# Performance work log

Hardware: AMD Instinct MI355X
Metric: run time of the kernel (lower is better)

The kernel has to match this reference:

```python
import jax, jax.numpy as jnp
import numpy as np

T, B, W, L = 64, 32, 1024, 4  # time, batch, hidden(=input) width, layers


def setup_inputs() -> dict:
    key = jax.random.key(0)
    ks = jax.random.split(key, 5)
    x = jax.random.normal(ks[0], (T, B, W), dtype=jnp.float32)
    resets = jax.random.randint(ks[1], (T, B), 0, 2).astype(bool)
    c0 = jnp.zeros((L, B, W), dtype=jnp.float32)
    h0 = jnp.zeros((L, B, W), dtype=jnp.float32)
    # Per-layer LSTM params (flax LSTMCell gate order: i, f, g, o concatenated).
    scale = 1.0 / np.sqrt(W)
    Wx = jax.random.normal(ks[2], (L, W, 4 * W), dtype=jnp.float32) * scale
    Wh = jax.random.normal(ks[3], (L, W, 4 * W), dtype=jnp.float32) * scale
    b = jnp.zeros((L, 4 * W), dtype=jnp.float32)
    return {"x": x, "resets": resets, "c0": c0, "h0": h0,
            "Wx": Wx, "Wh": Wh, "b": b}


def _lstm_scan(x, resets, c0, h0, Wx, Wh, b):
    num_layers = Wx.shape[0]

    def step(carry, xt):
        cs, hs = carry                      # each [L, B, W]
        ins, reset = xt                     # [B, W], [B]
        mask = reset[None, :, None]
        cs = jnp.where(mask, 0.0, cs)
        hs = jnp.where(mask, 0.0, hs)
        y = ins
        new_cs, new_hs = [], []
        for l in range(num_layers):
            gates = y @ Wx[l] + hs[l] @ Wh[l] + b[l]   # [B, 4W]
            i, f, g, o = jnp.split(gates, 4, axis=-1)
            c = jax.nn.sigmoid(f) * cs[l] + jax.nn.sigmoid(i) * jnp.tanh(g)
            h = jax.nn.sigmoid(o) * jnp.tanh(c)
            y = h
            new_cs.append(c)
            new_hs.append(h)
        return (jnp.stack(new_cs), jnp.stack(new_hs)), y

    (cs_f, hs_f), ys = jax.lax.scan(step, (c0, h0), (x, resets))
    return ys, cs_f, hs_f


def reference(x, resets, c0, h0, Wx, Wh, b):
    # ys: [T, B, W] stacked top-layer outputs; final carry also returned.
    return _lstm_scan(x, resets, c0, h0, Wx, Wh, b)
```

## Files before the change

### kernel.cpp

```cpp
#include <hip/hip_runtime.h>
#include <stdint.h>


typedef unsigned short u16;
typedef unsigned int u32;
typedef __attribute__((ext_vector_type(8))) short short8;
typedef __attribute__((ext_vector_type(4))) float f32x4;
typedef __attribute__((ext_vector_type(4))) unsigned int u32x4;

#define NT 64
#define NB 32
#define NW 1024
#define NLAY 4
#define G4 4096
#define POISON 0xAAAAAAAAu

#define HIST_OFF 0
#define RMASK_OFF 17104896
#define MODE_OFF 17113088

__device__ __forceinline__ float bf2f(u16 u) {
  union { u32 i; float f; } v; v.i = ((u32)u) << 16; return v.f;
}
__device__ __forceinline__ u16 f2bf(float f) {
  union { float f; u32 i; } v; v.f = f;
  u32 b = v.i;
  return (u16)((b + 0x7FFFu + ((b >> 16) & 1u)) >> 16);
}
__device__ __forceinline__ float sigmoidf_(float x) { return 1.f / (1.f + __expf(-x)); }
__device__ __forceinline__ float tanhfast(float x) {
  float cx = fminf(fmaxf(x, -15.f), 15.f);
  float e = __expf(2.f * cx);
  return (e - 1.f) / (e + 1.f);
}
union CastU { u32x4 u; short8 s; };
__device__ __forceinline__ short8 as_s8(u32x4 v) { CastU c; c.u = v; return c.s; }
__device__ __forceinline__ u32x4 as_u4(short8 v) { CastU c; c.s = v; return c.u; }

__device__ __forceinline__ void poll_half(const u16* rowA, const u16* rowB, u32x4 r[16]) {
  for (;;) {
#pragma unroll
    for (int q = 0; q < 8; ++q) {
      asm volatile("global_load_dwordx4 %0, %1, off sc0 sc1" : "=v"(r[q]) : "v"(rowA + q * 32));
      asm volatile("global_load_dwordx4 %0, %1, off sc0 sc1" : "=v"(r[8 + q]) : "v"(rowB + q * 32));
    }
    asm volatile("s_waitcnt vmcnt(0)"
                 : "+v"(r[0]), "+v"(r[1]), "+v"(r[2]), "+v"(r[3]), "+v"(r[4]), "+v"(r[5]),
                   "+v"(r[6]), "+v"(r[7]), "+v"(r[8]), "+v"(r[9]), "+v"(r[10]), "+v"(r[11]),
                   "+v"(r[12]), "+v"(r[13]), "+v"(r[14]), "+v"(r[15])
                 :
                 : "memory");
    bool ok = true;
    const u16* probe = rowA;
    bool have = false;
#pragma unroll
    for (int c = 0; c < 16; ++c) {
      bool f = (r[c].x != POISON) && (r[c].y != POISON) && (r[c].z != POISON) && (r[c].w != POISON);
      if (!f && !have) { probe = (c < 8) ? (rowA + c * 32) : (rowB + (c - 8) * 32); have = true; }
      ok &= f;
    }
    if (ok) return;
    for (;;) {
      __builtin_amdgcn_s_sleep(4);
      u32x4 v;
      asm volatile("global_load_dwordx4 %0, %1, off sc0 sc1" : "=v"(v) : "v"(probe));
      asm volatile("s_waitcnt vmcnt(0)" : "+v"(v) : : "memory");
      if ((v.x != POISON) && (v.y != POISON) && (v.z != POISON) && (v.w != POISON)) break;
    }
  }
}

__global__ void lstm_setup(const void* __restrict__ x, const void* __restrict__ resets,
                           int* __restrict__ modes, int* __restrict__ rmask) {
  __shared__ int votes_bf16, bad_int, bad_float;
  __shared__ int sm_rmode;
  int tid = threadIdx.x;
  if (tid == 0) { votes_bf16 = 0; bad_int = 0; bad_float = 0; }
  __syncthreads();
  {
    u32 w = ((const u32*)x)[tid];
    int e = (int)((w >> 7) & 0xFFu);
    if (e >= 100 && e <= 140) atomicAdd(&votes_bf16, 1);
  }
  if (tid < 128) {
    u32 r = ((const u32*)resets)[tid];
    if (r > 1u) atomicAdd(&bad_int, 1);
    if (r != 0u && r != 0x3F800000u) atomicAdd(&bad_float, 1);
  }
  __syncthreads();
  if (tid == 0) {
    int mbf = (votes_bf16 >= 192) ? 1 : 0;
    int rmode;
    if (bad_int == 0) rmode = 1;
    else if (bad_float == 0) rmode = 2;
    else rmode = 0;
    modes[0] = mbf;
    modes[1] = rmode;
    sm_rmode = rmode;
  }
  __syncthreads();
  int rmode = sm_rmode;
#pragma unroll
  for (int k = 0; k < 8; ++k) {
    int idx = tid * 8 + k;
    int val;
    if (rmode == 1) val = (((const int*)resets)[idx] != 0);
    else if (rmode == 2) val = (((const u32*)resets)[idx] != 0u);
    else val = (((const unsigned char*)resets)[idx] != 0);
    rmask[idx] = val;
  }
}

__global__ void lstm_poison(u32* __restrict__ hist32) {
  int g = (blockIdx.x * 256 + threadIdx.x) * 4;
  int l = g >> 20;
  int r = g & 1048575;
  u32x4 v = {POISON, POISON, POISON, POISON};
  *(u32x4*)(hist32 + ((size_t)l * 65 + 1) * 16384 + r) = v;
}

template <bool BF16>
__global__ void lstm_prep(const void* __restrict__ h0, const int* __restrict__ modes,
                          u16* __restrict__ hist) {
  if ((modes[0] != 0) != BF16) return;
  int idx = blockIdx.x * 256 + threadIdx.x;
  int l = idx >> 15;
  int rem = idx & 32767;
  float hv;
  if (BF16) hv = bf2f(((const u16*)h0)[idx]);
  else      hv = ((const float*)h0)[idx];
  hist[(size_t)l * (65 * NB * NW) + rem] = f2bf(hv);
}

template <bool BF16>
__global__ __launch_bounds__(256, 1) void lstm_main(
    const void* __restrict__ xv, const void* __restrict__ Wxv,
    const void* __restrict__ Whv, const void* __restrict__ biasv,
    const void* __restrict__ c0v,
    void* __restrict__ outv, const int* __restrict__ modes,
    const int* __restrict__ rmask, u16* __restrict__ hist) {
  if ((modes[0] != 0) != BF16) return;

  const int l = blockIdx.x >> 6;
  const int s = blockIdx.x & 63;
  const int hb = s * 16;
  const int tid = threadIdx.x;
  const int wave = tid >> 6;
  const int lane = tid & 63;
  const bool xpart = (wave < 2);
  const int krel = (wave & 1) * 512;
  const int lrow = lane & 15;
  const int lk8 = (lane >> 4) * 8;

  const int eb = tid >> 3;
  const int n0 = (tid & 7) * 2;
  const int emt = eb >> 4, er = eb & 15;

  __shared__ float red[4][2][4][16][17];

  short8 wfrag[4][16];
  {
    const size_t base = (size_t)l * NW * G4;
#pragma unroll
    for (int g = 0; g < 4; ++g) {
#pragma unroll
      for (int kt = 0; kt < 16; ++kt) {
        size_t off = base + (size_t)(krel + kt * 32 + lk8) * G4 + (size_t)(g * 1024 + hb + lrow);
        short8 v;
        if (BF16) {
          const u16* p = (xpart ? (const u16*)Wxv : (const u16*)Whv) + off;
#pragma unroll
          for (int j = 0; j < 8; ++j) v[j] = (short)p[(size_t)j * G4];
        } else {
          const float* p = (xpart ? (const float*)Wxv : (const float*)Whv) + off;
#pragma unroll
          for (int j = 0; j < 8; ++j) v[j] = (short)f2bf(p[(size_t)j * G4]);
        }
        wfrag[g][kt] = v;
      }
    }
  }

  float bias_r[4][2];
#pragma unroll
  for (int g = 0; g < 4; ++g)
#pragma unroll
    for (int j = 0; j < 2; ++j) {
      int bidx = l * G4 + g * 1024 + hb + n0 + j;
      bias_r[g][j] = BF16 ? bf2f(((const u16*)biasv)[bidx]) : ((const float*)biasv)[bidx];
    }

  float creg[2] = {0.f, 0.f};

#pragma unroll 1
  for (int t = 0; t < NT; ++t) {
    const u16* srcH = hist + ((size_t)l * 65 + t) * (NB * NW);
    const u16* srcY = hist + ((size_t)(l - 1) * 65 + (t + 1)) * (NB * NW);
    const u16* srcXb = (const u16*)xv + (size_t)t * NB * NW;
    const float* srcXf = (const float*)xv + (size_t)t * NB * NW;

    int rm0 = 0, rm1 = 0;
    if (!xpart) {
      rm0 = rmask[t * NB + lrow];
      rm1 = rmask[t * NB + 16 + lrow];
    }

    f32x4 acc[2][4];
    f32x4 zf = {0.f, 0.f, 0.f, 0.f};
#pragma unroll
    for (int mt = 0; mt < 2; ++mt)
#pragma unroll
      for (int g = 0; g < 4; ++g) acc[mt][g] = zf;

#pragma unroll
    for (int half = 0; half < 2; ++half) {
      u32x4 r[16];
      const int kbase = krel + half * 256 + lk8;
      if (xpart) {
        if (l > 0) {
          poll_half(srcY + (size_t)lrow * NW + kbase, srcY + (size_t)(lrow + 16) * NW + kbase, r);
        } else if (BF16) {
#pragma unroll
          for (int q = 0; q < 8; ++q) {
            r[q] = *(const u32x4*)(srcXb + (size_t)lrow * NW + kbase + q * 32);
            r[8 + q] = *(const u32x4*)(srcXb + (size_t)(lrow + 16) * NW + kbase + q * 32);
          }
        } else {
#pragma unroll
          for (int q = 0; q < 8; ++q) {
            const f32x4* p0 = (const f32x4*)(srcXf + (size_t)lrow * NW + kbase + q * 32);
            const f32x4* p1 = (const f32x4*)(srcXf + (size_t)(lrow + 16) * NW + kbase + q * 32);
            f32x4 x0a = p0[0], x0b = p0[1], x1a = p1[0], x1b = p1[1];
            short8 a0, a1;
#pragma unroll
            for (int j = 0; j < 4; ++j) {
              a0[j] = (short)f2bf(x0a[j]);
              a0[j + 4] = (short)f2bf(x0b[j]);
              a1[j] = (short)f2bf(x1a[j]);
              a1[j + 4] = (short)f2bf(x1b[j]);
            }
            r[q] = as_u4(a0);
            r[8 + q] = as_u4(a1);
          }
        }
      } else {
        poll_half(srcH + (size_t)lrow * NW + kbase, srcH + (size_t)(lrow + 16) * NW + kbase, r);
        u32x4 z4 = {0u, 0u, 0u, 0u};
        if (rm0) {
#pragma unroll
          for (int q = 0; q < 8; ++q) r[q] = z4;
        }
        if (rm1) {
#pragma unroll
          for (int q = 0; q < 8; ++q) r[8 + q] = z4;
        }
      }
#pragma unroll
      for (int q = 0; q < 8; ++q) {
        const int kt = half * 8 + q;
#pragma unroll
        for (int g = 0; g < 4; ++g) {
          acc[0][g] = __builtin_amdgcn_mfma_f32_16x16x32_bf16(as_s8(r[q]), wfrag[g][kt], acc[0][g], 0, 0, 0);
          acc[1][g] = __builtin_amdgcn_mfma_f32_16x16x32_bf16(as_s8(r[8 + q]), wfrag[g][kt], acc[1][g], 0, 0, 0);
        }
      }
    }

#pragma unroll
    for (int mt = 0; mt < 2; ++mt)
#pragma unroll
      for (int g = 0; g < 4; ++g)
#pragma unroll
        for (int r2 = 0; r2 < 4; ++r2)
          red[wave][mt][g][(lane >> 4) * 4 + r2][lrow] = acc[mt][g][r2];
    __syncthreads();

    {
      int rm = rmask[t * NB + eb];
      float hn[2];
#pragma unroll
      for (int j = 0; j < 2; ++j) {
        int n = n0 + j;
        float gv[4];
#pragma unroll
        for (int g = 0; g < 4; ++g)
          gv[g] = red[0][emt][g][er][n] + red[1][emt][g][er][n] +
                  red[2][emt][g][er][n] + red[3][emt][g][er][n] + bias_r[g][j];
        float c_old = creg[j];
        if (t == 0) {
          int cidx = (l * NB + eb) * NW + hb + n;
          c_old = BF16 ? bf2f(((const u16*)c0v)[cidx]) : ((const float*)c0v)[cidx];
        }
        if (rm) c_old = 0.f;
        float ci = sigmoidf_(gv[0]);
        float cf = sigmoidf_(gv[1]);
        float cg = tanhfast(gv[2]);
        float co = sigmoidf_(gv[3]);
        float cn = cf * c_old + ci * cg;
        hn[j] = co * tanhfast(cn);
        creg[j] = cn;
      }
      u32 hp = (u32)f2bf(hn[0]) | ((u32)f2bf(hn[1]) << 16);
      size_t hoff = ((size_t)l * 65 + (t + 1)) * (NB * NW) + (size_t)eb * NW + hb + n0;
      __hip_atomic_store((u32*)(hist + hoff), hp, __ATOMIC_RELAXED, __HIP_MEMORY_SCOPE_AGENT);
      if (l == NLAY - 1) {
        size_t oy = ((size_t)t * NB + eb) * NW + hb + n0;
        if (BF16) ((u32*)outv)[oy >> 1] = hp;
        else { ((float*)outv)[oy] = hn[0]; ((float*)outv)[oy + 1] = hn[1]; }
      }
      if (t == NT - 1) {
        size_t oc = (size_t)NT * NB * NW + ((size_t)l * NB + eb) * NW + hb + n0;
        size_t oh = oc + (size_t)NLAY * NB * NW;
        if (BF16) {
          u32 cp = (u32)f2bf(creg[0]) | ((u32)f2bf(creg[1]) << 16);
          ((u32*)outv)[oc >> 1] = cp;
          ((u32*)outv)[oh >> 1] = hp;
        } else {
          ((float*)outv)[oc] = creg[0];
          ((float*)outv)[oc + 1] = creg[1];
          ((float*)outv)[oh] = hn[0];
          ((float*)outv)[oh + 1] = hn[1];
        }
      }
    }
    __syncthreads();
  }
}

extern "C" void kernel_launch(void* const* d_in, const int* in_sizes, int n_in,
                              void* d_out, int out_size, void* d_ws, size_t ws_size,
                              hipStream_t stream) {
  const void* x = d_in[0];
  const void* resets = d_in[1];
  const void* c0 = d_in[2];
  const void* h0 = d_in[3];
  const void* Wx = d_in[4];
  const void* Wh = d_in[5];
  const void* bias = d_in[6];

  char* ws = (char*)d_ws;
  u16* hist = (u16*)(ws + HIST_OFF);
  int* rmask = (int*)(ws + RMASK_OFF);
  int* modes = (int*)(ws + MODE_OFF);

  lstm_setup<<<1, 256, 0, stream>>>(x, resets, modes, rmask);
  lstm_poison<<<4096, 256, 0, stream>>>((u32*)hist);
  lstm_prep<true><<<512, 256, 0, stream>>>(h0, modes, hist);
  lstm_prep<false><<<512, 256, 0, stream>>>(h0, modes, hist);
  lstm_main<true><<<256, 256, 0, stream>>>(x, Wx, Wh, bias, c0, d_out, modes, rmask, hist);
  lstm_main<false><<<256, 256, 0, stream>>>(x, Wx, Wh, bias, c0, d_out, modes, rmask, hist);
}
```

Baseline: 1.035 ms.

## Replace poison-value data polling with per-block ready flags

Each block now publishes a per-timestep ready flag after its hidden-state stores have completed. Consumer waves spin on the 32 flags covering their K-slice before doing a single plain load of the history data, instead of repeatedly reloading the data and checking it for a poison sentinel. This removes the separate kernel that filled the history buffer with poison and cuts redundant wide reloads while spinning. The cost is an extra dependent round trip on the recurrent critical path: producers must store, wait, barrier and then set the flag, and consumers must see the flag before loading.

After: 1.096 ms. +5.8%, slower.

```diff
diff --git a/kernel.cpp b/kernel.cpp
--- a/kernel.cpp
+++ b/kernel.cpp
@@ -13,11 +13,12 @@
 #define NW 1024
 #define NLAY 4
 #define G4 4096
-#define POISON 0xAAAAAAAAu
 
 #define HIST_OFF 0
 #define RMASK_OFF 17104896
 #define MODE_OFF 17113088
+#define FLAG_OFF 17113344
+#define FLAG_PER_L 4160
 
 __device__ __forceinline__ float bf2f(u16 u) {
   union { u32 i; float f; } v; v.i = ((u32)u) << 16; return v.f;
@@ -37,41 +38,33 @@
 __device__ __forceinline__ short8 as_s8(u32x4 v) { CastU c; c.u = v; return c.s; }
 __device__ __forceinline__ u32x4 as_u4(short8 v) { CastU c; c.s = v; return c.u; }
 
-__device__ __forceinline__ void poll_half(const u16* rowA, const u16* rowB, u32x4 r[16]) {
+__device__ __forceinline__ void load_half(const u16* rowA, const u16* rowB, u32x4 r[16]) {
+#pragma unroll
+  for (int q = 0; q < 8; ++q) {
+    asm volatile("global_load_dwordx4 %0, %1, off sc0 sc1" : "=v"(r[q]) : "v"(rowA + q * 32));
+    asm volatile("global_load_dwordx4 %0, %1, off sc0 sc1" : "=v"(r[8 + q]) : "v"(rowB + q * 32));
+  }
+  asm volatile("s_waitcnt vmcnt(0)"
+               : "+v"(r[0]), "+v"(r[1]), "+v"(r[2]), "+v"(r[3]), "+v"(r[4]), "+v"(r[5]),
+                 "+v"(r[6]), "+v"(r[7]), "+v"(r[8]), "+v"(r[9]), "+v"(r[10]), "+v"(r[11]),
+                 "+v"(r[12]), "+v"(r[13]), "+v"(r[14]), "+v"(r[15])
+               :
+               : "memory");
+}
+
+__device__ __forceinline__ void poll_ready(const u32* fp) {
   for (;;) {
-#pragma unroll
-    for (int q = 0; q < 8; ++q) {
-      asm volatile("global_load_dwordx4 %0, %1, off sc0 sc1" : "=v"(r[q]) : "v"(rowA + q * 32));
-      asm volatile("global_load_dwordx4 %0, %1, off sc0 sc1" : "=v"(r[8 + q]) : "v"(rowB + q * 32));
-    }
-    asm volatile("s_waitcnt vmcnt(0)"
-                 : "+v"(r[0]), "+v"(r[1]), "+v"(r[2]), "+v"(r[3]), "+v"(r[4]), "+v"(r[5]),
-                   "+v"(r[6]), "+v"(r[7]), "+v"(r[8]), "+v"(r[9]), "+v"(r[10]), "+v"(r[11]),
-                   "+v"(r[12]), "+v"(r[13]), "+v"(r[14]), "+v"(r[15])
-                 :
-                 : "memory");
-    bool ok = true;
-    const u16* probe = rowA;
-    bool have = false;
-#pragma unroll
-    for (int c = 0; c < 16; ++c) {
-      bool f = (r[c].x != POISON) && (r[c].y != POISON) && (r[c].z != POISON) && (r[c].w != POISON);
-      if (!f && !have) { probe = (c < 8) ? (rowA + c * 32) : (rowB + (c - 8) * 32); have = true; }
-      ok &= f;
-    }
-    if (ok) return;
-    for (;;) {
-      __builtin_amdgcn_s_sleep(4);
-      u32x4 v;
-      asm volatile("global_load_dwordx4 %0, %1, off sc0 sc1" : "=v"(v) : "v"(probe));
-      asm volatile("s_waitcnt vmcnt(0)" : "+v"(v) : : "memory");
-      if ((v.x != POISON) && (v.y != POISON) && (v.z != POISON) && (v.w != POISON)) break;
-    }
+    u32 f;
+    asm volatile("global_load_dword %0, %1, off sc0 sc1" : "=v"(f) : "v"(fp));
+    asm volatile("s_waitcnt vmcnt(0)" : "+v"(f) : : "memory");
+    if (__all(f != 0)) return;
+    __builtin_amdgcn_s_sleep(1);
   }
 }
 
 __global__ void lstm_setup(const void* __restrict__ x, const void* __restrict__ resets,
-                           int* __restrict__ modes, int* __restrict__ rmask) {
+                           int* __restrict__ modes, int* __restrict__ rmask,
+                           u32* __restrict__ flags) {
   __shared__ int votes_bf16, bad_int, bad_float;
   __shared__ int sm_rmode;
   int tid = threadIdx.x;
@@ -109,14 +102,9 @@
     else val = (((const unsigned char*)resets)[idx] != 0);
     rmask[idx] = val;
   }
-}
-
-__global__ void lstm_poison(u32* __restrict__ hist32) {
-  int g = (blockIdx.x * 256 + threadIdx.x) * 4;
-  int l = g >> 20;
-  int r = g & 1048575;
-  u32x4 v = {POISON, POISON, POISON, POISON};
-  *(u32x4*)(hist32 + ((size_t)l * 65 + 1) * 16384 + r) = v;
+  for (int i = 0; i < 65; ++i) flags[tid * 65 + i] = 0;
+  __syncthreads();
+  flags[(tid >> 6) * FLAG_PER_L + (tid & 63)] = 1;
 }
 
 template <bool BF16>
@@ -138,7 +126,8 @@
     const void* __restrict__ Whv, const void* __restrict__ biasv,
     const void* __restrict__ c0v,
     void* __restrict__ outv, const int* __restrict__ modes,
-    const int* __restrict__ rmask, u16* __restrict__ hist) {
+    const int* __restrict__ rmask, u16* __restrict__ hist,
+    u32* __restrict__ flags) {
   if ((modes[0] != 0) != BF16) return;
 
   const int l = blockIdx.x >> 6;
@@ -158,6 +147,11 @@
 
   __shared__ float red[4][2][4][16][17];
 
+  const u32* fpoll = xpart ? (l > 0 ? flags + (size_t)(l - 1) * FLAG_PER_L : nullptr)
+                           : flags + (size_t)l * FLAG_PER_L;
+  const int fslice = (krel >> 4) + (lane & 31);
+  u32* fset = flags + (size_t)l * FLAG_PER_L + 64 + s;
+
   short8 wfrag[4][16];
   {
     const size_t base = (size_t)l * NW * G4;
@@ -205,6 +199,12 @@
       rm1 = rmask[t * NB + 16 + lrow];
     }
 
+    if (xpart) {
+      if (l > 0) poll_ready(fpoll + (size_t)(t + 1) * 64 + fslice);
+    } else {
+      poll_ready(fpoll + (size_t)t * 64 + fslice);
+    }
+
     f32x4 acc[2][4];
     f32x4 zf = {0.f, 0.f, 0.f, 0.f};
 #pragma unroll
@@ -218,7 +218,7 @@
       const int kbase = krel + half * 256 + lk8;
       if (xpart) {
         if (l > 0) {
-          poll_half(srcY + (size_t)lrow * NW + kbase, srcY + (size_t)(lrow + 16) * NW + kbase, r);
+          load_half(srcY + (size_t)lrow * NW + kbase, srcY + (size_t)(lrow + 16) * NW + kbase, r);
         } else if (BF16) {
 #pragma unroll
           for (int q = 0; q < 8; ++q) {
@@ -244,7 +244,7 @@
           }
         }
       } else {
-        poll_half(srcH + (size_t)lrow * NW + kbase, srcH + (size_t)(lrow + 16) * NW + kbase, r);
+        load_half(srcH + (size_t)lrow * NW + kbase, srcH + (size_t)(lrow + 16) * NW + kbase, r);
         u32x4 z4 = {0u, 0u, 0u, 0u};
         if (rm0) {
 #pragma unroll
@@ -275,6 +275,7 @@
           red[wave][mt][g][(lane >> 4) * 4 + r2][lrow] = acc[mt][g][r2];
     __syncthreads();
 
+    u32 hp;
     {
       int rm = rmask[t * NB + eb];
       float hn[2];
@@ -300,9 +301,10 @@
         hn[j] = co * tanhfast(cn);
         creg[j] = cn;
       }
-      u32 hp = (u32)f2bf(hn[0]) | ((u32)f2bf(hn[1]) << 16);
+      hp = (u32)f2bf(hn[0]) | ((u32)f2bf(hn[1]) << 16);
       size_t hoff = ((size_t)l * 65 + (t + 1)) * (NB * NW) + (size_t)eb * NW + hb + n0;
-      __hip_atomic_store((u32*)(hist + hoff), hp, __ATOMIC_RELAXED, __HIP_MEMORY_SCOPE_AGENT);
+      u32* hptr = (u32*)(hist + hoff);
+      asm volatile("global_store_dword %0, %1, off sc0 sc1" : : "v"(hptr), "v"(hp) : "memory");
       if (l == NLAY - 1) {
         size_t oy = ((size_t)t * NB + eb) * NW + hb + n0;
         if (BF16) ((u32*)outv)[oy >> 1] = hp;
@@ -323,7 +325,13 @@
         }
       }
     }
+
+    asm volatile("s_waitcnt vmcnt(0)" : : : "memory");
     __syncthreads();
+    if (tid == 0) {
+      asm volatile("global_store_dword %0, %1, off sc0 sc1" : : "v"(fset), "v"(1u) : "memory");
+    }
+    fset += 64;
   }
 }
 
@@ -342,11 +350,11 @@
   u16* hist = (u16*)(ws + HIST_OFF);
   int* rmask = (int*)(ws + RMASK_OFF);
   int* modes = (int*)(ws + MODE_OFF);
-
-  lstm_setup<<<1, 256, 0, stream>>>(x, resets, modes, rmask);
-  lstm_poison<<<4096, 256, 0, stream>>>((u32*)hist);
+  u32* flags = (u32*)(ws + FLAG_OFF);
+
+  lstm_setup<<<1, 256, 0, stream>>>(x, resets, modes, rmask, flags);
   lstm_prep<true><<<512, 256, 0, stream>>>(h0, modes, hist);
   lstm_prep<false><<<512, 256, 0, stream>>>(h0, modes, hist);
-  lstm_main<true><<<256, 256, 0, stream>>>(x, Wx, Wh, bias, c0, d_out, modes, rmask, hist);
-  lstm_main<false><<<256, 256, 0, stream>>>(x, Wx, Wh, bias, c0, d_out, modes, rmask, hist);
-}
+  lstm_main<true><<<256, 256, 0, stream>>>(x, Wx, Wh, bias, c0, d_out, modes, rmask, hist, flags);
+  lstm_main<false><<<256, 256, 0, stream>>>(x, Wx, Wh, bias, c0, d_out, modes, rmask, hist, flags);
+}
```

## Double-buffer reduction LDS and retry only stale chunks when polling

Applied to the files above, without the earlier changes.

The LDS reduction buffer is double-buffered by timestep parity, which lets the trailing __syncthreads at the end of each timestep be removed so waves can start polling the next step earlier. The polling routine now keeps a per-chunk stale bitmask and reloads only the chunks that are still stale, instead of reloading all chunks after a single-probe sleep loop. It sleeps only when every chunk is stale and uses wave-wide votes for loop exit. This shortens the latency on the recurrent critical path, at the cost of twice the LDS and reliance on the double buffer to avoid write-after-read races between steps.

After: 1.052 ms. Within noise of the previous version (+1.6%).

```diff
diff --git a/kernel.cpp b/kernel.cpp
--- a/kernel.cpp
+++ b/kernel.cpp
@@ -37,35 +37,42 @@
 __device__ __forceinline__ short8 as_s8(u32x4 v) { CastU c; c.u = v; return c.s; }
 __device__ __forceinline__ u32x4 as_u4(short8 v) { CastU c; c.s = v; return c.u; }
 
+__device__ __forceinline__ bool fresh4(u32x4 v) {
+  return (v.x != POISON) && (v.y != POISON) && (v.z != POISON) && (v.w != POISON);
+}
+
+#define WAITCNT_ALL(r)                                                                        \
+  asm volatile("s_waitcnt vmcnt(0)"                                                           \
+               : "+v"(r[0]), "+v"(r[1]), "+v"(r[2]), "+v"(r[3]), "+v"(r[4]), "+v"(r[5]),      \
+                 "+v"(r[6]), "+v"(r[7]), "+v"(r[8]), "+v"(r[9]), "+v"(r[10]), "+v"(r[11]),    \
+                 "+v"(r[12]), "+v"(r[13]), "+v"(r[14]), "+v"(r[15])                           \
+               :                                                                              \
+               : "memory")
+
 __device__ __forceinline__ void poll_half(const u16* rowA, const u16* rowB, u32x4 r[16]) {
-  for (;;) {
-#pragma unroll
-    for (int q = 0; q < 8; ++q) {
-      asm volatile("global_load_dwordx4 %0, %1, off sc0 sc1" : "=v"(r[q]) : "v"(rowA + q * 32));
-      asm volatile("global_load_dwordx4 %0, %1, off sc0 sc1" : "=v"(r[8 + q]) : "v"(rowB + q * 32));
-    }
-    asm volatile("s_waitcnt vmcnt(0)"
-                 : "+v"(r[0]), "+v"(r[1]), "+v"(r[2]), "+v"(r[3]), "+v"(r[4]), "+v"(r[5]),
-                   "+v"(r[6]), "+v"(r[7]), "+v"(r[8]), "+v"(r[9]), "+v"(r[10]), "+v"(r[11]),
-                   "+v"(r[12]), "+v"(r[13]), "+v"(r[14]), "+v"(r[15])
-                 :
-                 : "memory");
-    bool ok = true;
-    const u16* probe = rowA;
-    bool have = false;
+#pragma unroll
+  for (int q = 0; q < 8; ++q) {
+    asm volatile("global_load_dwordx4 %0, %1, off sc0 sc1" : "=v"(r[q]) : "v"(rowA + q * 32));
+    asm volatile("global_load_dwordx4 %0, %1, off sc0 sc1" : "=v"(r[8 + q]) : "v"(rowB + q * 32));
+  }
+  WAITCNT_ALL(r);
+  u32 stale = 0;
+#pragma unroll
+  for (int c = 0; c < 16; ++c)
+    if (!fresh4(r[c])) stale |= (1u << c);
+  while (__any(stale != 0)) {
+    if (__all(stale == 0xFFFFu)) __builtin_amdgcn_s_sleep(2);
 #pragma unroll
     for (int c = 0; c < 16; ++c) {
-      bool f = (r[c].x != POISON) && (r[c].y != POISON) && (r[c].z != POISON) && (r[c].w != POISON);
-      if (!f && !have) { probe = (c < 8) ? (rowA + c * 32) : (rowB + (c - 8) * 32); have = true; }
-      ok &= f;
-    }
-    if (ok) return;
-    for (;;) {
-      __builtin_amdgcn_s_sleep(4);
-      u32x4 v;
-      asm volatile("global_load_dwordx4 %0, %1, off sc0 sc1" : "=v"(v) : "v"(probe));
-      asm volatile("s_waitcnt vmcnt(0)" : "+v"(v) : : "memory");
-      if ((v.x != POISON) && (v.y != POISON) && (v.z != POISON) && (v.w != POISON)) break;
+      if (stale & (1u << c)) {
+        const u16* p = (c < 8) ? (rowA + c * 32) : (rowB + (c - 8) * 32);
+        asm volatile("global_load_dwordx4 %0, %1, off sc0 sc1" : "=v"(r[c]) : "v"(p));
+      }
+    }
+    WAITCNT_ALL(r);
+#pragma unroll
+    for (int c = 0; c < 16; ++c) {
+      if ((stale & (1u << c)) && fresh4(r[c])) stale &= ~(1u << c);
     }
   }
 }
@@ -156,7 +163,7 @@
   const int n0 = (tid & 7) * 2;
   const int emt = eb >> 4, er = eb & 15;
 
-  __shared__ float red[4][2][4][16][17];
+  __shared__ float red[2][4][2][4][16][17];
 
   short8 wfrag[4][16];
   {
@@ -194,6 +201,7 @@
 
 #pragma unroll 1
   for (int t = 0; t < NT; ++t) {
+    const int buf = t & 1;
     const u16* srcH = hist + ((size_t)l * 65 + t) * (NB * NW);
     const u16* srcY = hist + ((size_t)(l - 1) * 65 + (t + 1)) * (NB * NW);
     const u16* srcXb = (const u16*)xv + (size_t)t * NB * NW;
@@ -272,7 +280,7 @@
       for (int g = 0; g < 4; ++g)
 #pragma unroll
         for (int r2 = 0; r2 < 4; ++r2)
-          red[wave][mt][g][(lane >> 4) * 4 + r2][lrow] = acc[mt][g][r2];
+          red[buf][wave][mt][g][(lane >> 4) * 4 + r2][lrow] = acc[mt][g][r2];
     __syncthreads();
 
     {
@@ -284,8 +292,8 @@
         float gv[4];
 #pragma unroll
         for (int g = 0; g < 4; ++g)
-          gv[g] = red[0][emt][g][er][n] + red[1][emt][g][er][n] +
-                  red[2][emt][g][er][n] + red[3][emt][g][er][n] + bias_r[g][j];
+          gv[g] = red[buf][0][emt][g][er][n] + red[buf][1][emt][g][er][n] +
+                  red[buf][2][emt][g][er][n] + red[buf][3][emt][g][er][n] + bias_r[g][j];
         float c_old = creg[j];
         if (t == 0) {
           int cidx = (l * NB + eb) * NW + hb + n;
@@ -323,7 +331,6 @@
         }
       }
     }
-    __syncthreads();
   }
 }
 
```

## Decouple input-projection and recurrent waves with LDS flag pipeline

Applied to the files above, without the earlier changes.

Splits each block into two wave groups: the y/x-projection waves run ahead through timesteps independently, writing partial sums into double-buffered LDS slots and signalling via LDS counters. The h-recurrent waves compute the Wh product, wait for both partial sums, and do the elementwise cell update, replacing the per-step block-wide barriers. This lets the input-projection GEMM for step t+1 overlap the recurrent critical path. It adds spin-wait flag synchronization with memory-ordering risk and uses different poll sleep intervals for the two groups.

Result: slower. 1.086 ms (+4.9%).

```diff
diff --git a/kernel.cpp b/kernel.cpp
--- a/kernel.cpp
+++ b/kernel.cpp
@@ -37,6 +37,22 @@
 __device__ __forceinline__ short8 as_s8(u32x4 v) { CastU c; c.u = v; return c.s; }
 __device__ __forceinline__ u32x4 as_u4(short8 v) { CastU c; c.s = v; return c.u; }
 
+__device__ __forceinline__ bool fresh4(u32x4 v) {
+  return (v.x != POISON) && (v.y != POISON) && (v.z != POISON) && (v.w != POISON);
+}
+
+__device__ __forceinline__ void lds_bump(int* p) {
+  __threadfence_block();
+  if ((threadIdx.x & 63) == 0)
+    __hip_atomic_fetch_add(p, 1, __ATOMIC_RELAXED, __HIP_MEMORY_SCOPE_WORKGROUP);
+}
+__device__ __forceinline__ void lds_wait(int* p, int want) {
+  while (__hip_atomic_load(p, __ATOMIC_RELAXED, __HIP_MEMORY_SCOPE_WORKGROUP) < want)
+    __builtin_amdgcn_s_sleep(1);
+  __threadfence_block();
+}
+
+template <int SLP>
 __device__ __forceinline__ void poll_half(const u16* rowA, const u16* rowB, u32x4 r[16]) {
   for (;;) {
 #pragma unroll
@@ -61,7 +77,7 @@
     }
     if (ok) return;
     for (;;) {
-      __builtin_amdgcn_s_sleep(4);
+      __builtin_amdgcn_s_sleep(SLP);
       u32x4 v;
       asm volatile("global_load_dwordx4 %0, %1, off sc0 sc1" : "=v"(v) : "v"(probe));
       asm volatile("s_waitcnt vmcnt(0)" : "+v"(v) : : "memory");
@@ -147,16 +163,16 @@
   const int tid = threadIdx.x;
   const int wave = tid >> 6;
   const int lane = tid & 63;
-  const bool xpart = (wave < 2);
+  const bool ypart = (wave < 2);
   const int krel = (wave & 1) * 512;
   const int lrow = lane & 15;
   const int lk8 = (lane >> 4) * 8;
 
-  const int eb = tid >> 3;
-  const int n0 = (tid & 7) * 2;
-  const int emt = eb >> 4, er = eb & 15;
-
-  __shared__ float red[4][2][4][16][17];
+  __shared__ float yred[2][2][2][4][16][17];
+  __shared__ float hred[2][2][2][4][16][17];
+  __shared__ int yflag, hflag, edone;
+
+  if (tid == 0) { yflag = 0; hflag = 0; edone = 0; }
 
   short8 wfrag[4][16];
   {
@@ -168,11 +184,11 @@
         size_t off = base + (size_t)(krel + kt * 32 + lk8) * G4 + (size_t)(g * 1024 + hb + lrow);
         short8 v;
         if (BF16) {
-          const u16* p = (xpart ? (const u16*)Wxv : (const u16*)Whv) + off;
+          const u16* p = (ypart ? (const u16*)Wxv : (const u16*)Whv) + off;
 #pragma unroll
           for (int j = 0; j < 8; ++j) v[j] = (short)p[(size_t)j * G4];
         } else {
-          const float* p = (xpart ? (const float*)Wxv : (const float*)Whv) + off;
+          const float* p = (ypart ? (const float*)Wxv : (const float*)Whv) + off;
 #pragma unroll
           for (int j = 0; j < 8; ++j) v[j] = (short)f2bf(p[(size_t)j * G4]);
         }
@@ -180,45 +196,29 @@
       }
     }
   }
-
-  float bias_r[4][2];
-#pragma unroll
-  for (int g = 0; g < 4; ++g)
-#pragma unroll
-    for (int j = 0; j < 2; ++j) {
-      int bidx = l * G4 + g * 1024 + hb + n0 + j;
-      bias_r[g][j] = BF16 ? bf2f(((const u16*)biasv)[bidx]) : ((const float*)biasv)[bidx];
-    }
-
-  float creg[2] = {0.f, 0.f};
-
+  __syncthreads();
+
+  if (ypart) {
 #pragma unroll 1
-  for (int t = 0; t < NT; ++t) {
-    const u16* srcH = hist + ((size_t)l * 65 + t) * (NB * NW);
-    const u16* srcY = hist + ((size_t)(l - 1) * 65 + (t + 1)) * (NB * NW);
-    const u16* srcXb = (const u16*)xv + (size_t)t * NB * NW;
-    const float* srcXf = (const float*)xv + (size_t)t * NB * NW;
-
-    int rm0 = 0, rm1 = 0;
-    if (!xpart) {
-      rm0 = rmask[t * NB + lrow];
-      rm1 = rmask[t * NB + 16 + lrow];
-    }
-
-    f32x4 acc[2][4];
-    f32x4 zf = {0.f, 0.f, 0.f, 0.f};
-#pragma unroll
-    for (int mt = 0; mt < 2; ++mt)
-#pragma unroll
-      for (int g = 0; g < 4; ++g) acc[mt][g] = zf;
-
-#pragma unroll
-    for (int half = 0; half < 2; ++half) {
-      u32x4 r[16];
-      const int kbase = krel + half * 256 + lk8;
-      if (xpart) {
+    for (int t = 0; t < NT; ++t) {
+      const int slot = t & 1;
+      const u16* srcY = hist + ((size_t)(l - 1) * 65 + (t + 1)) * (NB * NW);
+      const u16* srcXb = (const u16*)xv + (size_t)t * NB * NW;
+      const float* srcXf = (const float*)xv + (size_t)t * NB * NW;
+
+      f32x4 acc[2][4];
+      f32x4 zf = {0.f, 0.f, 0.f, 0.f};
+#pragma unroll
+      for (int mt = 0; mt < 2; ++mt)
+#pragma unroll
+        for (int g = 0; g < 4; ++g) acc[mt][g] = zf;
+
+#pragma unroll
+      for (int half = 0; half < 2; ++half) {
+        u32x4 r[16];
+        const int kbase = krel + half * 256 + lk8;
         if (l > 0) {
-          poll_half(srcY + (size_t)lrow * NW + kbase, srcY + (size_t)(lrow + 16) * NW + kbase, r);
+          poll_half<16>(srcY + (size_t)lrow * NW + kbase, srcY + (size_t)(lrow + 16) * NW + kbase, r);
         } else if (BF16) {
 #pragma unroll
           for (int q = 0; q < 8; ++q) {
@@ -243,8 +243,64 @@
             r[8 + q] = as_u4(a1);
           }
         }
-      } else {
-        poll_half(srcH + (size_t)lrow * NW + kbase, srcH + (size_t)(lrow + 16) * NW + kbase, r);
+#pragma unroll
+        for (int q = 0; q < 8; ++q) {
+          const int kt = half * 8 + q;
+#pragma unroll
+          for (int g = 0; g < 4; ++g) {
+            acc[0][g] = __builtin_amdgcn_mfma_f32_16x16x32_bf16(as_s8(r[q]), wfrag[g][kt], acc[0][g], 0, 0, 0);
+            acc[1][g] = __builtin_amdgcn_mfma_f32_16x16x32_bf16(as_s8(r[8 + q]), wfrag[g][kt], acc[1][g], 0, 0, 0);
+          }
+        }
+      }
+
+      if (t >= 2) lds_wait(&edone, 2 * (t - 1));
+#pragma unroll
+      for (int mt = 0; mt < 2; ++mt)
+#pragma unroll
+        for (int g = 0; g < 4; ++g)
+#pragma unroll
+          for (int e = 0; e < 4; ++e)
+            yred[slot][wave][mt][g][(lane >> 4) * 4 + e][lrow] = acc[mt][g][e];
+      lds_bump(&yflag);
+    }
+  } else {
+    const int hw = wave - 2;
+    const int tid2 = tid - 128;
+    const int eb = tid2 >> 2;
+    const int eu = (tid2 & 3) * 4;
+    const int emt = eb >> 4, er = eb & 15;
+
+    float bias_r[4][4];
+#pragma unroll
+    for (int g = 0; g < 4; ++g)
+#pragma unroll
+      for (int j = 0; j < 4; ++j) {
+        int bidx = l * G4 + g * 1024 + hb + eu + j;
+        bias_r[g][j] = BF16 ? bf2f(((const u16*)biasv)[bidx]) : ((const float*)biasv)[bidx];
+      }
+
+    float creg[4] = {0.f, 0.f, 0.f, 0.f};
+
+#pragma unroll 1
+    for (int t = 0; t < NT; ++t) {
+      const int slot = t & 1;
+      const u16* srcH = hist + ((size_t)l * 65 + t) * (NB * NW);
+      int rm0 = rmask[t * NB + lrow];
+      int rm1 = rmask[t * NB + 16 + lrow];
+
+      f32x4 acc[2][4];
+      f32x4 zf = {0.f, 0.f, 0.f, 0.f};
+#pragma unroll
+      for (int mt = 0; mt < 2; ++mt)
+#pragma unroll
+        for (int g = 0; g < 4; ++g) acc[mt][g] = zf;
+
+#pragma unroll
+      for (int half = 0; half < 2; ++half) {
+        u32x4 r[16];
+        const int kbase = krel + half * 256 + lk8;
+        poll_half<4>(srcH + (size_t)lrow * NW + kbase, srcH + (size_t)(lrow + 16) * NW + kbase, r);
         u32x4 z4 = {0u, 0u, 0u, 0u};
         if (rm0) {
 #pragma unroll
@@ -254,76 +310,90 @@
 #pragma unroll
           for (int q = 0; q < 8; ++q) r[8 + q] = z4;
         }
+#pragma unroll
+        for (int q = 0; q < 8; ++q) {
+          const int kt = half * 8 + q;
+#pragma unroll
+          for (int g = 0; g < 4; ++g) {
+            acc[0][g] = __builtin_amdgcn_mfma_f32_16x16x32_bf16(as_s8(r[q]), wfrag[g][kt], acc[0][g], 0, 0, 0);
+            acc[1][g] = __builtin_amdgcn_mfma_f32_16x16x32_bf16(as_s8(r[8 + q]), wfrag[g][kt], acc[1][g], 0, 0, 0);
+          }
+        }
       }
-#pragma unroll
-      for (int q = 0; q < 8; ++q) {
-        const int kt = half * 8 + q;
-#pragma unroll
-        for (int g = 0; g < 4; ++g) {
-          acc[0][g] = __builtin_amdgcn_mfma_f32_16x16x32_bf16(as_s8(r[q]), wfrag[g][kt], acc[0][g], 0, 0, 0);
-          acc[1][g] = __builtin_amdgcn_mfma_f32_16x16x32_bf16(as_s8(r[8 + q]), wfrag[g][kt], acc[1][g], 0, 0, 0);
+
+      if (t >= 2) lds_wait(&edone, 2 * (t - 1));
+#pragma unroll
+      for (int mt = 0; mt < 2; ++mt)
+#pragma unroll
+        for (int g = 0; g < 4; ++g)
+#pragma unroll
+          for (int e = 0; e < 4; ++e)
+            hred[slot][hw][mt][g][(lane >> 4) * 4 + e][lrow] = acc[mt][g][e];
+      lds_bump(&hflag);
+
+      lds_wait(&hflag, 2 * (t + 1));
+      lds_wait(&yflag, 2 * (t + 1));
+
+      {
+        int rm = rmask[t * NB + eb];
+        float hn[4];
+#pragma unroll
+        for (int j = 0; j < 4; ++j) {
+          int n = eu + j;
+          float gv[4];
+#pragma unroll
+          for (int g = 0; g < 4; ++g)
+            gv[g] = yred[slot][0][emt][g][er][n] + yred[slot][1][emt][g][er][n] +
+                    hred[slot][0][emt][g][er][n] + hred[slot][1][emt][g][er][n] + bias_r[g][j];
+          float c_old = creg[j];
+          if (t == 0) {
+            int cidx = (l * NB + eb) * NW + hb + n;
+            c_old = BF16 ? bf2f(((const u16*)c0v)[cidx]) : ((const float*)c0v)[cidx];
+          }
+          if (rm) c_old = 0.f;
+          float ci = sigmoidf_(gv[0]);
+          float cf = sigmoidf_(gv[1]);
+          float cg = tanhfast(gv[2]);
+          float co = sigmoidf_(gv[3]);
+          float cn = cf * c_old + ci * cg;
+          hn[j] = co * tanhfast(cn);
+          creg[j] = cn;
+        }
+        u32 hp0 = (u32)f2bf(hn[0]) | ((u32)f2bf(hn[1]) << 16);
+        u32 hp1 = (u32)f2bf(hn[2]) | ((u32)f2bf(hn[3]) << 16);
+        size_t hoff = ((size_t)l * 65 + (t + 1)) * (NB * NW) + (size_t)eb * NW + hb + eu;
+        u32* hptr = (u32*)(hist + hoff);
+        __hip_atomic_store(hptr, hp0, __ATOMIC_RELAXED, __HIP_MEMORY_SCOPE_AGENT);
+        __hip_atomic_store(hptr + 1, hp1, __ATOMIC_RELAXED, __HIP_MEMORY_SCOPE_AGENT);
+        if (l == NLAY - 1) {
+          size_t oy = ((size_t)t * NB + eb) * NW + hb + eu;
+          if (BF16) {
+            ((u32*)outv)[oy >> 1] = hp0;
+            ((u32*)outv)[(oy >> 1) + 1] = hp1;
+          } else {
+            float* op = (float*)outv + oy;
+            op[0] = hn[0]; op[1] = hn[1]; op[2] = hn[2]; op[3] = hn[3];
+          }
+        }
+        if (t == NT - 1) {
+          size_t oc = (size_t)NT * NB * NW + ((size_t)l * NB + eb) * NW + hb + eu;
+          size_t oh = oc + (size_t)NLAY * NB * NW;
+          if (BF16) {
+            u32 cp0 = (u32)f2bf(creg[0]) | ((u32)f2bf(creg[1]) << 16);
+            u32 cp1 = (u32)f2bf(creg[2]) | ((u32)f2bf(creg[3]) << 16);
+            ((u32*)outv)[oc >> 1] = cp0;
+            ((u32*)outv)[(oc >> 1) + 1] = cp1;
+            ((u32*)outv)[oh >> 1] = hp0;
+            ((u32*)outv)[(oh >> 1) + 1] = hp1;
+          } else {
+            float* ov = (float*)outv;
+            ov[oc + 0] = creg[0]; ov[oc + 1] = creg[1]; ov[oc + 2] = creg[2]; ov[oc + 3] = creg[3];
+            ov[oh + 0] = hn[0]; ov[oh + 1] = hn[1]; ov[oh + 2] = hn[2]; ov[oh + 3] = hn[3];
+          }
         }
       }
-    }
-
-#pragma unroll
-    for (int mt = 0; mt < 2; ++mt)
-#pragma unroll
-      for (int g = 0; g < 4; ++g)
-#pragma unroll
-        for (int r2 = 0; r2 < 4; ++r2)
-          red[wave][mt][g][(lane >> 4) * 4 + r2][lrow] = acc[mt][g][r2];
-    __syncthreads();
-
-    {
-      int rm = rmask[t * NB + eb];
-      float hn[2];
-#pragma unroll
-      for (int j = 0; j < 2; ++j) {
-        int n = n0 + j;
-        float gv[4];
-#pragma unroll
-        for (int g = 0; g < 4; ++g)
-          gv[g] = red[0][emt][g][er][n] + red[1][emt][g][er][n] +
-                  red[2][emt][g][er][n] + red[3][emt][g][er][n] + bias_r[g][j];
-        float c_old = creg[j];
-        if (t == 0) {
-          int cidx = (l * NB + eb) * NW + hb + n;
-          c_old = BF16 ? bf2f(((const u16*)c0v)[cidx]) : ((const float*)c0v)[cidx];
-        }
-        if (rm) c_old = 0.f;
-        float ci = sigmoidf_(gv[0]);
-        float cf = sigmoidf_(gv[1]);
-        float cg = tanhfast(gv[2]);
-        float co = sigmoidf_(gv[3]);
-        float cn = cf * c_old + ci * cg;
-        hn[j] = co * tanhfast(cn);
-        creg[j] = cn;
-      }
-      u32 hp = (u32)f2bf(hn[0]) | ((u32)f2bf(hn[1]) << 16);
-      size_t hoff = ((size_t)l * 65 + (t + 1)) * (NB * NW) + (size_t)eb * NW + hb + n0;
-      __hip_atomic_store((u32*)(hist + hoff), hp, __ATOMIC_RELAXED, __HIP_MEMORY_SCOPE_AGENT);
-      if (l == NLAY - 1) {
-        size_t oy = ((size_t)t * NB + eb) * NW + hb + n0;
-        if (BF16) ((u32*)outv)[oy >> 1] = hp;
-        else { ((float*)outv)[oy] = hn[0]; ((float*)outv)[oy + 1] = hn[1]; }
-      }
-      if (t == NT - 1) {
-        size_t oc = (size_t)NT * NB * NW + ((size_t)l * NB + eb) * NW + hb + n0;
-        size_t oh = oc + (size_t)NLAY * NB * NW;
-        if (BF16) {
-          u32 cp = (u32)f2bf(creg[0]) | ((u32)f2bf(creg[1]) << 16);
-          ((u32*)outv)[oc >> 1] = cp;
-          ((u32*)outv)[oh >> 1] = hp;
-        } else {
-          ((float*)outv)[oc] = creg[0];
-          ((float*)outv)[oc + 1] = creg[1];
-          ((float*)outv)[oh] = hn[0];
-          ((float*)outv)[oh + 1] = hn[1];
-        }
-      }
-    }
-    __syncthreads();
+      lds_bump(&edone);
+    }
   }
 }
 
```
